# Optimization experiments

Hardware: AMD Instinct MI355X
Metric: run time of the kernel (lower is better)

Reference implementation:

```python
import jax, jax.numpy as jnp
import numpy as np

H, W, PS = 256, 128, 16
NPH, NPW = H // PS, W // PS          # 16, 8
P = NPH * NPW                        # 128 patches
D = PS * PS                          # 256 patch dim
HID = 1024 // P                      # 8 hidden per patch


def setup_inputs() -> dict:
    key = jax.random.key(0)
    k1, k2, k3, k4, k5 = jax.random.split(key, 5)
    x = jax.random.normal(k1, (4, 512, H * W), dtype=jnp.float32)
    # per-patch locally-connected weights (grouped 1x1 conv == batched small GEMM)
    We = jax.random.normal(k2, (P, HID, D), dtype=jnp.float32) * (1.0 / np.sqrt(D))
    be = jax.random.normal(k3, (P, HID), dtype=jnp.float32) * 0.01
    Wd = jax.random.normal(k4, (P, D, HID), dtype=jnp.float32) * (1.0 / np.sqrt(HID))
    bd = jax.random.normal(k5, (P, D), dtype=jnp.float32) * 0.01
    return {"x": x, "We": We, "be": be, "Wd": Wd, "bd": bd}


def reference(x, We, be, Wd, bd):
    B, S, _ = x.shape
    N = B * S
    # extract non-overlapping 16x16 patches: [N, P=128, D=256]
    xp = x.reshape(N, NPH, PS, NPW, PS).transpose(0, 1, 3, 2, 4).reshape(N, P, D)
    # per-patch encode: 128 independent (256 -> 8) linears
    z = jnp.einsum('npd,phd->nph', xp, We) + be          # [N, P, HID]
    # per-patch decode: 128 independent (8 -> 256) linears
    dec = jnp.einsum('nph,pdh->npd', z, Wd) + bd         # [N, P, D]
    # reassemble patches back to [B, S, H*W]
    out = dec.reshape(N, NPH, NPW, PS, PS).transpose(0, 1, 3, 2, 4).reshape(B, S, H * W)
    return jax.nn.sigmoid(out)
```

## Files before the change

### kernel.cpp

```cpp
#include <hip/hip_runtime.h>

#define HH 256
#define WW 128
#define DD 256
#define HID 8
#define G 16
#define NP2 (G / 2)
#define PSTRIDE 272
#define ZSTR 16
#define IMG (HH * WW)

typedef float v4f __attribute__((ext_vector_type(4)));

__device__ __forceinline__ void pl32swap(float& a, float& b) {
    asm("v_permlane32_swap_b32 %0, %1" : "+v"(a), "+v"(b));
}
__device__ __forceinline__ void pl16swap(float& a, float& b) {
    asm("v_permlane16_swap_b32 %0, %1" : "+v"(a), "+v"(b));
}
template <int CTRL>
__device__ __forceinline__ float dpp_get(float v) {
    return __int_as_float(__builtin_amdgcn_update_dpp(
        0, __float_as_int(v), CTRL, 0xf, 0xf, true));
}
#define DPP_QUAD_XOR1 177
#define DPP_QUAD_XOR2 78
#define DPP_ROW_ROR8  0x128
#define DPP_HALF_MIRR 0x141

__global__ __launch_bounds__(512, 4)
void lca_kernel(const float* __restrict__ x, const float* __restrict__ We,
                const float* __restrict__ be, const float* __restrict__ Wd,
                const float* __restrict__ bd, float* __restrict__ out) {
    __shared__ float Xb[2][2][8 * PSTRIDE];
    __shared__ float Zb[2][2][8 * ZSTR];

    const int bid = blockIdx.x;
    const int ph  = bid & 15;
    const int sg  = bid >> 4;
    const int tid = threadIdx.x;
    const int w   = tid >> 6;
    const int l   = tid & 63;
    const int p_w = ph * 8 + w;

    const int r_t  = tid >> 5;
    const int pw_t = (tid >> 2) & 7;
    const int jj_t = (tid & 3) * 4;
    const int lds_stage = pw_t * PSTRIDE + r_t * 16 + jj_t;
    const int goff = tid * 4;
    const int p_t  = ph * 8 + pw_t;
    const int d_t  = r_t * 16 + jj_t;

    v4f we4[HID];
#pragma unroll
    for (int h = 0; h < HID; ++h)
        we4[h] = *(const v4f*)(We + ((size_t)(p_w * HID + h)) * DD + l * 4);
    const float bew = be[p_w * HID + (l >> 3)];

    v4f wd4[4][2];
#pragma unroll
    for (int c = 0; c < 4; ++c) {
        const v4f* wp = (const v4f*)(Wd + ((size_t)(p_t * DD + d_t + c)) * HID);
        wd4[c][0] = wp[0];
        wd4[c][1] = wp[1];
    }
    v4f bdv = *(const v4f*)(bd + p_t * DD + d_t);

    const bool b3 = (l & 8) != 0;

    const float* xs = x   + (size_t)(sg * G) * IMG + ph * 2048;
    float*       os = out + (size_t)(sg * G) * IMG + ph * 2048;

    {
        v4f a0 = *(const v4f*)(xs + goff);
        v4f a1 = *(const v4f*)(xs + IMG + goff);
        *(v4f*)&Xb[0][0][lds_stage] = a0;
        *(v4f*)&Xb[0][1][lds_stage] = a1;
    }

#pragma unroll 1
    for (int q = 0; q < NP2; ++q) {
        __syncthreads();

        v4f xr0, xr1;
        if (q + 1 < NP2) {
            xr0 = *(const v4f*)(xs + (size_t)(2 * q + 2) * IMG + goff);
            xr1 = *(const v4f*)(xs + (size_t)(2 * q + 3) * IMG + goff);
        }

        if (q > 0) {
#pragma unroll
            for (int ss = 0; ss < 2; ++ss) {
                const float* zp = &Zb[(q - 1) & 1][ss][pw_t * ZSTR];
                v4f z0 = *(const v4f*)zp;
                v4f z1 = *(const v4f*)(zp + 4);
                v4f o;
#pragma unroll
                for (int c = 0; c < 4; ++c) {
                    float acc = bdv[c];
#pragma unroll
                    for (int h = 0; h < 4; ++h) acc = fmaf(wd4[c][0][h], z0[h], acc);
#pragma unroll
                    for (int h = 0; h < 4; ++h) acc = fmaf(wd4[c][1][h], z1[h], acc);
                    o[c] = __builtin_amdgcn_rcpf(1.0f + __expf(-acc));
                }
                __builtin_nontemporal_store(
                    o, (v4f*)(os + (size_t)(2 * (q - 1) + ss) * IMG + goff));
            }
        }

#pragma unroll
        for (int ss = 0; ss < 2; ++ss) {
            v4f xv = *(const v4f*)&Xb[q & 1][ss][w * PSTRIDE + 4 * l];
            float z[HID];
#pragma unroll
            for (int h = 0; h < HID; ++h)
                z[h] = fmaf(we4[h].x, xv.x,
                       fmaf(we4[h].y, xv.y,
                       fmaf(we4[h].z, xv.z, we4[h].w * xv.w)));

            pl32swap(z[0], z[4]); float a0 = z[0] + z[4];
            pl32swap(z[1], z[5]); float a1 = z[1] + z[5];
            pl32swap(z[2], z[6]); float a2 = z[2] + z[6];
            pl32swap(z[3], z[7]); float a3 = z[3] + z[7];
            pl16swap(a0, a2); float c0 = a0 + a2;
            pl16swap(a1, a3); float c1 = a1 + a3;
            float keep = b3 ? c1 : c0;
            float send = b3 ? c0 : c1;
            float s1 = keep + dpp_get<DPP_ROW_ROR8>(send);
            s1 += dpp_get<DPP_QUAD_XOR1>(s1);
            s1 += dpp_get<DPP_QUAD_XOR2>(s1);
            s1 += dpp_get<DPP_HALF_MIRR>(s1);

            if ((l & 7) == 0)
                Zb[q & 1][ss][w * ZSTR + (l >> 3)] = s1 + bew;
        }

        if (q + 1 < NP2) {
            *(v4f*)&Xb[(q + 1) & 1][0][lds_stage] = xr0;
            *(v4f*)&Xb[(q + 1) & 1][1][lds_stage] = xr1;
        }
    }

    __syncthreads();
#pragma unroll
    for (int ss = 0; ss < 2; ++ss) {
        const float* zp = &Zb[(NP2 - 1) & 1][ss][pw_t * ZSTR];
        v4f z0 = *(const v4f*)zp;
        v4f z1 = *(const v4f*)(zp + 4);
        v4f o;
#pragma unroll
        for (int c = 0; c < 4; ++c) {
            float acc = bdv[c];
#pragma unroll
            for (int h = 0; h < 4; ++h) acc = fmaf(wd4[c][0][h], z0[h], acc);
#pragma unroll
            for (int h = 0; h < 4; ++h) acc = fmaf(wd4[c][1][h], z1[h], acc);
            o[c] = __builtin_amdgcn_rcpf(1.0f + __expf(-acc));
        }
        __builtin_nontemporal_store(
            o, (v4f*)(os + (size_t)(2 * (NP2 - 1) + ss) * IMG + goff));
    }
}

extern "C" void kernel_launch(void* const* d_in, const int* in_sizes, int n_in,
                              void* d_out, int out_size, void* d_ws, size_t ws_size,
                              hipStream_t stream) {
    const float* x  = (const float*)d_in[0];
    const float* We = (const float*)d_in[1];
    const float* be = (const float*)d_in[2];
    const float* Wd = (const float*)d_in[3];
    const float* bd = (const float*)d_in[4];
    float* out = (float*)d_out;

    const int n_total = in_sizes[0] / IMG;
    const int grid    = 16 * (n_total / G);
    lca_kernel<<<dim3(grid), dim3(512), 0, stream>>>(x, We, be, Wd, bd, out);
}
```

Measured before the change: 95.65 us.

## Encode directly from global-load layout, dropping LDS transpose of x

Threads now compute encoder partial sums on x exactly as it arrives from global memory, so the staging of x through LDS for a transpose is removed. Partial sums are reduced within quads and across wave halves, written to LDS per wave, then summed across the 8 waves by a finalize step. A three-stage software pipeline (encode, finalize, decode) shares the single barrier per iteration. This trades LDS traffic for x for more cross-lane reduction work and an extra cross-wave sum pass.

```diff
diff --git a/kernel.cpp b/kernel.cpp
--- a/kernel.cpp
+++ b/kernel.cpp
@@ -6,17 +6,12 @@
 #define HID 8
 #define G 16
 #define NP2 (G / 2)
-#define PSTRIDE 272
-#define ZSTR 16
 #define IMG (HH * WW)
 
 typedef float v4f __attribute__((ext_vector_type(4)));
 
 __device__ __forceinline__ void pl32swap(float& a, float& b) {
     asm("v_permlane32_swap_b32 %0, %1" : "+v"(a), "+v"(b));
-}
-__device__ __forceinline__ void pl16swap(float& a, float& b) {
-    asm("v_permlane16_swap_b32 %0, %1" : "+v"(a), "+v"(b));
 }
 template <int CTRL>
 __device__ __forceinline__ float dpp_get(float v) {
@@ -25,15 +20,13 @@
 }
 #define DPP_QUAD_XOR1 177
 #define DPP_QUAD_XOR2 78
-#define DPP_ROW_ROR8  0x128
-#define DPP_HALF_MIRR 0x141
 
 __global__ __launch_bounds__(512, 4)
 void lca_kernel(const float* __restrict__ x, const float* __restrict__ We,
                 const float* __restrict__ be, const float* __restrict__ Wd,
                 const float* __restrict__ bd, float* __restrict__ out) {
-    __shared__ float Xb[2][2][8 * PSTRIDE];
-    __shared__ float Zb[2][2][8 * ZSTR];
+    __shared__ float Zp[2][2][8][64];
+    __shared__ float Zf[2][2][64];
 
     const int bid = blockIdx.x;
     const int ph  = bid & 15;
@@ -41,126 +34,115 @@
     const int tid = threadIdx.x;
     const int w   = tid >> 6;
     const int l   = tid & 63;
-    const int p_w = ph * 8 + w;
-
-    const int r_t  = tid >> 5;
-    const int pw_t = (tid >> 2) & 7;
-    const int jj_t = (tid & 3) * 4;
-    const int lds_stage = pw_t * PSTRIDE + r_t * 16 + jj_t;
+    const int p   = (tid >> 2) & 7;
+    const int r   = tid >> 5;
+    const int d0  = r * 16 + 4 * (tid & 3);
+    const int pg  = ph * 8 + p;
     const int goff = tid * 4;
-    const int p_t  = ph * 8 + pw_t;
-    const int d_t  = r_t * 16 + jj_t;
 
     v4f we4[HID];
 #pragma unroll
     for (int h = 0; h < HID; ++h)
-        we4[h] = *(const v4f*)(We + ((size_t)(p_w * HID + h)) * DD + l * 4);
-    const float bew = be[p_w * HID + (l >> 3)];
+        we4[h] = *(const v4f*)(We + ((size_t)(pg * HID + h)) * DD + d0);
 
     v4f wd4[4][2];
 #pragma unroll
     for (int c = 0; c < 4; ++c) {
-        const v4f* wp = (const v4f*)(Wd + ((size_t)(p_t * DD + d_t + c)) * HID);
+        const v4f* wp = (const v4f*)(Wd + ((size_t)(pg * DD + d0 + c)) * HID);
         wd4[c][0] = wp[0];
         wd4[c][1] = wp[1];
     }
-    v4f bdv = *(const v4f*)(bd + p_t * DD + d_t);
+    v4f bdv = *(const v4f*)(bd + pg * DD + d0);
 
-    const bool b3 = (l & 8) != 0;
+    float bef = 0.f;
+    if (tid < 128)
+        bef = be[(ph * 8 + ((tid >> 3) & 7)) * HID + (tid & 7)];
 
     const float* xs = x   + (size_t)(sg * G) * IMG + ph * 2048;
     float*       os = out + (size_t)(sg * G) * IMG + ph * 2048;
 
-    {
-        v4f a0 = *(const v4f*)(xs + goff);
-        v4f a1 = *(const v4f*)(xs + IMG + goff);
-        *(v4f*)&Xb[0][0][lds_stage] = a0;
-        *(v4f*)&Xb[0][1][lds_stage] = a1;
-    }
+    const bool writer = (l & 3) == 0;
+    const int  par    = l >> 5;
+
+    auto encode = [&](const v4f& xv, int buf, int ss) {
+        float pt[HID];
+#pragma unroll
+        for (int h = 0; h < HID; ++h)
+            pt[h] = fmaf(we4[h].x, xv.x,
+                    fmaf(we4[h].y, xv.y,
+                    fmaf(we4[h].z, xv.z, we4[h].w * xv.w)));
+#pragma unroll
+        for (int h = 0; h < HID; ++h) {
+            pt[h] += dpp_get<DPP_QUAD_XOR1>(pt[h]);
+            pt[h] += dpp_get<DPP_QUAD_XOR2>(pt[h]);
+        }
+        pl32swap(pt[0], pt[1]); float s0 = pt[0] + pt[1];
+        pl32swap(pt[2], pt[3]); float s1 = pt[2] + pt[3];
+        pl32swap(pt[4], pt[5]); float s2 = pt[4] + pt[5];
+        pl32swap(pt[6], pt[7]); float s3 = pt[6] + pt[7];
+        if (writer) {
+            v4f v = {s0, s1, s2, s3};
+            *(v4f*)&Zp[buf][ss][w][p * 8 + par * 4] = v;
+        }
+    };
+
+    auto finalize = [&](int j) {
+        if (tid < 128) {
+            const int s  = tid >> 6;
+            const int pp = (tid >> 3) & 7;
+            const int hh = tid & 7;
+            const float* zp0 = &Zp[j & 1][s][0][pp * 8 + (hh & 1) * 4 + (hh >> 1)];
+            float acc = bef;
+#pragma unroll
+            for (int w8 = 0; w8 < 8; ++w8) acc += zp0[w8 * 64];
+            Zf[j & 1][s][pp * 8 + hh] = acc;
+        }
+    };
+
+    auto decode = [&](int j) {
+#pragma unroll
+        for (int ss = 0; ss < 2; ++ss) {
+            const float* zp = &Zf[j & 1][ss][p * 8];
+            v4f z0 = *(const v4f*)zp;
+            v4f z1 = *(const v4f*)(zp + 4);
+            v4f o;
+#pragma unroll
+            for (int c = 0; c < 4; ++c) {
+                float acc = bdv[c];
+#pragma unroll
+                for (int h = 0; h < 4; ++h) acc = fmaf(wd4[c][0][h], z0[h], acc);
+#pragma unroll
+                for (int h = 0; h < 4; ++h) acc = fmaf(wd4[c][1][h], z1[h], acc);
+                o[c] = __builtin_amdgcn_rcpf(1.0f + __expf(-acc));
+            }
+            __builtin_nontemporal_store(
+                o, (v4f*)(os + (size_t)(2 * j + ss) * IMG + goff));
+        }
+    };
+
+    v4f xv0 = *(const v4f*)(xs + goff);
+    v4f xv1 = *(const v4f*)(xs + IMG + goff);
 
 #pragma unroll 1
     for (int q = 0; q < NP2; ++q) {
         __syncthreads();
-
         v4f xr0, xr1;
         if (q + 1 < NP2) {
             xr0 = *(const v4f*)(xs + (size_t)(2 * q + 2) * IMG + goff);
             xr1 = *(const v4f*)(xs + (size_t)(2 * q + 3) * IMG + goff);
         }
-
-        if (q > 0) {
-#pragma unroll
-            for (int ss = 0; ss < 2; ++ss) {
-                const float* zp = &Zb[(q - 1) & 1][ss][pw_t * ZSTR];
-                v4f z0 = *(const v4f*)zp;
-                v4f z1 = *(const v4f*)(zp + 4);
-                v4f o;
-#pragma unroll
-                for (int c = 0; c < 4; ++c) {
-                    float acc = bdv[c];
-#pragma unroll
-                    for (int h = 0; h < 4; ++h) acc = fmaf(wd4[c][0][h], z0[h], acc);
-#pragma unroll
-                    for (int h = 0; h < 4; ++h) acc = fmaf(wd4[c][1][h], z1[h], acc);
-                    o[c] = __builtin_amdgcn_rcpf(1.0f + __expf(-acc));
-                }
-                __builtin_nontemporal_store(
-                    o, (v4f*)(os + (size_t)(2 * (q - 1) + ss) * IMG + goff));
-            }
-        }
-
-#pragma unroll
-        for (int ss = 0; ss < 2; ++ss) {
-            v4f xv = *(const v4f*)&Xb[q & 1][ss][w * PSTRIDE + 4 * l];
-            float z[HID];
-#pragma unroll
-            for (int h = 0; h < HID; ++h)
-                z[h] = fmaf(we4[h].x, xv.x,
-                       fmaf(we4[h].y, xv.y,
-                       fmaf(we4[h].z, xv.z, we4[h].w * xv.w)));
-
-            pl32swap(z[0], z[4]); float a0 = z[0] + z[4];
-            pl32swap(z[1], z[5]); float a1 = z[1] + z[5];
-            pl32swap(z[2], z[6]); float a2 = z[2] + z[6];
-            pl32swap(z[3], z[7]); float a3 = z[3] + z[7];
-            pl16swap(a0, a2); float c0 = a0 + a2;
-            pl16swap(a1, a3); float c1 = a1 + a3;
-            float keep = b3 ? c1 : c0;
-            float send = b3 ? c0 : c1;
-            float s1 = keep + dpp_get<DPP_ROW_ROR8>(send);
-            s1 += dpp_get<DPP_QUAD_XOR1>(s1);
-            s1 += dpp_get<DPP_QUAD_XOR2>(s1);
-            s1 += dpp_get<DPP_HALF_MIRR>(s1);
-
-            if ((l & 7) == 0)
-                Zb[q & 1][ss][w * ZSTR + (l >> 3)] = s1 + bew;
-        }
-
-        if (q + 1 < NP2) {
-            *(v4f*)&Xb[(q + 1) & 1][0][lds_stage] = xr0;
-            *(v4f*)&Xb[(q + 1) & 1][1][lds_stage] = xr1;
-        }
+        if (q >= 2) decode(q - 2);
+        encode(xv0, q & 1, 0);
+        encode(xv1, q & 1, 1);
+        if (q >= 1) finalize(q - 1);
+        xv0 = xr0; xv1 = xr1;
     }
 
     __syncthreads();
-#pragma unroll
-    for (int ss = 0; ss < 2; ++ss) {
-        const float* zp = &Zb[(NP2 - 1) & 1][ss][pw_t * ZSTR];
-        v4f z0 = *(const v4f*)zp;
-        v4f z1 = *(const v4f*)(zp + 4);
-        v4f o;
-#pragma unroll
-        for (int c = 0; c < 4; ++c) {
-            float acc = bdv[c];
-#pragma unroll
-            for (int h = 0; h < 4; ++h) acc = fmaf(wd4[c][0][h], z0[h], acc);
-#pragma unroll
-            for (int h = 0; h < 4; ++h) acc = fmaf(wd4[c][1][h], z1[h], acc);
-            o[c] = __builtin_amdgcn_rcpf(1.0f + __expf(-acc));
-        }
-        __builtin_nontemporal_store(
-            o, (v4f*)(os + (size_t)(2 * (NP2 - 1) + ss) * IMG + goff));
-    }
+    finalize(NP2 - 1);
+    decode(NP2 - 2);
+    __syncthreads();
+    decode(NP2 - 1);
 }
 
 extern "C" void kernel_launch(void* const* d_in, const int* in_sizes, int n_in,
```

Result: slower. 97.96 us (+2.4%).
